# Optimization experiments

Hardware: AMD Instinct MI355X
Metric: run time of the kernel (lower is better)

## Reference

```python
import jax, jax.numpy as jnp
import numpy as np

TEMPERATURE = 0.1
EPS = 1e-8  # torch cosine_similarity eps
NEG_FILL = -9e15

def setup_inputs() -> dict:
    key = jax.random.key(0)
    stacked_batch = jax.random.normal(key, (8192, 128), dtype=jnp.float32)
    return {"stacked_batch": stacked_batch}

def reference(stacked_batch) -> jnp.ndarray:
    n = stacked_batch.shape[0]
    # cosine similarity = normalized GEMM (equivalent to torch broadcast form)
    norm = jnp.maximum(jnp.linalg.norm(stacked_batch, axis=-1, keepdims=True), EPS)
    z = stacked_batch / norm                      # [N, D]
    sim = jnp.matmul(z, z.T) / TEMPERATURE        # [N, N]
    # mask self-similarity on the diagonal
    idx = jnp.arange(n)
    sim = sim.at[idx, idx].set(NEG_FILL)
    # positive pair for row i is column (i + N/2) mod N
    pos_cols = (idx + n // 2) % n
    pos = sim[idx, pos_cols]                      # [N]
    loss = jax.scipy.special.logsumexp(sim, axis=-1) - pos
    return loss.mean()
```

## Files before the change

### kernel.cpp

```cpp
#include <hip/hip_runtime.h>
#include <hip/hip_bf16.h>

#define N 8192
#define D 128
#define HALF_N 4096
#define SQRT_SCALE_LOG2E 3.79828236f
#define LN2 0.693147180559945f

#define BLOCK_ROWS 256
#define COLS_PER_ITER 64
#define COL_SPLITS 16
#define COLS_PER_BLOCK (N / COL_SPLITS)
#define ITERS (COLS_PER_BLOCK / COLS_PER_ITER)
#define LDS_STRIDE 136

typedef short frag8 __attribute__((ext_vector_type(8)));
typedef float f32x4 __attribute__((ext_vector_type(4)));

#define OFF_POS    0
#define OFF_PSUMS  (N)
#define OFF_ACC    (N + COL_SPLITS * N)
#define OFF_CNT    (OFF_ACC + 1)
#define OFF_Z_BYTES ((OFF_ACC + 64) * 4)

__device__ __forceinline__ unsigned short f2bf(float f) {
    unsigned int u = __float_as_uint(f);
    u += 0x7FFFu + ((u >> 16) & 1u);
    return (unsigned short)(u >> 16);
}

__global__ __launch_bounds__(256) void k_normalize(const float* __restrict__ x,
                                                   unsigned short* __restrict__ z,
                                                   float* __restrict__ acc0,
                                                   unsigned int* __restrict__ counter) {
    const int row  = blockIdx.x * 4 + (threadIdx.x >> 6);
    const int lane = threadIdx.x & 63;
    float2 v = ((const float2*)x)[row * 64 + lane];
    float s = v.x * v.x + v.y * v.y;
    #pragma unroll
    for (int m = 32; m >= 1; m >>= 1) s += __shfl_xor(s, m);
    float inv = SQRT_SCALE_LOG2E / fmaxf(sqrtf(s), 1e-8f);
    ushort2 o;
    o.x = f2bf(v.x * inv);
    o.y = f2bf(v.y * inv);
    ((ushort2*)z)[row * 64 + lane] = o;
    if (blockIdx.x == 0 && threadIdx.x == 0) { acc0[0] = 0.0f; counter[0] = 0u; }
}

__global__ __launch_bounds__(256, 2) void k_simloss(const unsigned short* __restrict__ z,
                                                    float* __restrict__ psums,
                                                    float* __restrict__ pos) {
    __shared__ unsigned short lds[COLS_PER_ITER * LDS_STRIDE];

    const int tid  = threadIdx.x;
    const int wave = tid >> 6;
    const int lane = tid & 63;
    const int l15  = lane & 15;
    const int quad = lane >> 4;
    const int wrow = blockIdx.x * BLOCK_ROWS + wave * 64;
    const int colbase0 = blockIdx.y * COLS_PER_BLOCK;
    const int posbase  = (wrow + HALF_N) & (N - 1);

    const int st_r  = tid >> 4;
    const int st_c8 = tid & 15;

    frag8 a[4][4];
    #pragma unroll
    for (int s = 0; s < 4; ++s) {
        const uint4* p = (const uint4*)&z[(wrow + s * 16 + l15) * D + quad * 8];
        #pragma unroll
        for (int q = 0; q < 4; ++q) {
            uint4 t = p[q * 4];
            a[s][q] = *(frag8*)&t;
        }
    }

    float sums[4][4];
    #pragma unroll
    for (int s = 0; s < 4; ++s)
        #pragma unroll
        for (int r = 0; r < 4; ++r) sums[s][r] = 0.0f;

    uint4 t[4];
    #pragma unroll
    for (int u = 0; u < 4; ++u)
        t[u] = *(const uint4*)&z[(colbase0 + u * 16 + st_r) * D + st_c8 * 8];

    for (int it = 0; it < ITERS; ++it) {
        const int colbase = colbase0 + it * COLS_PER_ITER;
        __syncthreads();
        #pragma unroll
        for (int u = 0; u < 4; ++u)
            *(uint4*)&lds[(u * 16 + st_r) * LDS_STRIDE + st_c8 * 8] = t[u];
        __syncthreads();

        if (it + 1 < ITERS) {
            const int nb = colbase + COLS_PER_ITER;
            #pragma unroll
            for (int u = 0; u < 4; ++u)
                t[u] = *(const uint4*)&z[(nb + u * 16 + st_r) * D + st_c8 * 8];
        }

        const bool isDiag = (colbase == wrow);
        const bool isPos  = (colbase == posbase);
        const unsigned short* lp = &lds[l15 * LDS_STRIDE + quad * 8];

        #pragma unroll
        for (int c = 0; c < 4; ++c) {
            f32x4 acc[4];
            #pragma unroll
            for (int s = 0; s < 4; ++s) acc[s] = (f32x4){0.f, 0.f, 0.f, 0.f};
            #pragma unroll
            for (int q = 0; q < 4; ++q) {
                frag8 b = *(const frag8*)(lp + c * 16 * LDS_STRIDE + q * 32);
                #pragma unroll
                for (int s = 0; s < 4; ++s)
                    acc[s] = __builtin_amdgcn_mfma_f32_16x16x32_bf16(a[s][q], b, acc[s], 0, 0, 0);
            }
            if (isDiag | isPos) {
                #pragma unroll
                for (int s = 0; s < 4; ++s)
                    #pragma unroll
                    for (int r = 0; r < 4; ++r) {
                        float v = acc[s][r];
                        float e = __builtin_amdgcn_exp2f(v);
                        if (c == s) {
                            bool hit = (l15 == quad * 4 + r);
                            if (isDiag && hit) e = 0.0f;
                            if (isPos  && hit) pos[wrow + s * 16 + quad * 4 + r] = v * LN2;
                        }
                        sums[s][r] += e;
                    }
            } else {
                #pragma unroll
                for (int s = 0; s < 4; ++s)
                    #pragma unroll
                    for (int r = 0; r < 4; ++r)
                        sums[s][r] += __builtin_amdgcn_exp2f(acc[s][r]);
            }
        }
    }

    #pragma unroll
    for (int s = 0; s < 4; ++s)
        #pragma unroll
        for (int r = 0; r < 4; ++r) {
            float v = sums[s][r];
            v += __shfl_xor(v, 1);
            v += __shfl_xor(v, 2);
            v += __shfl_xor(v, 4);
            v += __shfl_xor(v, 8);
            if (l15 == 0)
                psums[blockIdx.y * N + wrow + s * 16 + quad * 4 + r] = v;
        }
}

__global__ __launch_bounds__(256) void k_rowloss(const float* __restrict__ psums,
                                                 const float* __restrict__ pos,
                                                 float* __restrict__ acc0,
                                                 unsigned int* __restrict__ counter,
                                                 float* __restrict__ out) {
    const int row = blockIdx.x * 256 + threadIdx.x;
    float t = 0.0f;
    #pragma unroll
    for (int s = 0; s < COL_SPLITS; ++s) t += psums[s * N + row];
    float loss = __logf(t) - pos[row];
    #pragma unroll
    for (int m = 32; m >= 1; m >>= 1) loss += __shfl_xor(loss, m);
    __shared__ float p[4];
    if ((threadIdx.x & 63) == 0) p[threadIdx.x >> 6] = loss;
    __syncthreads();
    if (threadIdx.x == 0) {
        atomicAdd(acc0, p[0] + p[1] + p[2] + p[3]);
        __threadfence();
        unsigned prev = atomicAdd(counter, 1u);
        if (prev == gridDim.x - 1) {
            float total = atomicAdd(acc0, 0.0f);
            out[0] = total * (1.0f / N);
        }
    }
}

extern "C" void kernel_launch(void* const* d_in, const int* in_sizes, int n_in,
                              void* d_out, int out_size, void* d_ws, size_t ws_size,
                              hipStream_t stream) {
    const float* x = (const float*)d_in[0];
    float* wsf   = (float*)d_ws;
    float* pos   = wsf + OFF_POS;
    float* psums = wsf + OFF_PSUMS;
    float* acc0  = wsf + OFF_ACC;
    unsigned int* counter = (unsigned int*)(wsf + OFF_CNT);
    unsigned short* z = (unsigned short*)((char*)d_ws + OFF_Z_BYTES);

    k_normalize<<<N / 4, 256, 0, stream>>>(x, z, acc0, counter);
    dim3 g2(N / BLOCK_ROWS, COL_SPLITS);
    k_simloss<<<g2, 256, 0, stream>>>(z, psums, pos);
    k_rowloss<<<N / 256, 256, 0, stream>>>(psums, pos, acc0, counter, (float*)d_out);
}
```

Baseline: 90.95 us.

## Exploit similarity matrix symmetry with triangular tiling and column-sum atomics

Launches only upper-triangular 256x128 tiles of the symmetric similarity matrix and accumulates both row and column exp-sums via atomics, roughly halving the GEMM and exp work. The 16-way column-split partial-sum buffer is replaced by a single atomically accumulated sum vector, zeroed in the normalize kernel. Positive logits are stored only for the first half of the rows and reused by symmetry. Adds many float atomics and drops register prefetch of the next column tile, and makes the summation order nondeterministic.

```diff
diff --git a/kernel.cpp b/kernel.cpp
--- a/kernel.cpp
+++ b/kernel.cpp
@@ -7,21 +7,18 @@
 #define SQRT_SCALE_LOG2E 3.79828236f
 #define LN2 0.693147180559945f
 
-#define BLOCK_ROWS 256
 #define COLS_PER_ITER 64
-#define COL_SPLITS 16
-#define COLS_PER_BLOCK (N / COL_SPLITS)
-#define ITERS (COLS_PER_BLOCK / COLS_PER_ITER)
+#define ITERS 2
 #define LDS_STRIDE 136
 
 typedef short frag8 __attribute__((ext_vector_type(8)));
 typedef float f32x4 __attribute__((ext_vector_type(4)));
 
-#define OFF_POS    0
-#define OFF_PSUMS  (N)
-#define OFF_ACC    (N + COL_SPLITS * N)
-#define OFF_CNT    (OFF_ACC + 1)
-#define OFF_Z_BYTES ((OFF_ACC + 64) * 4)
+#define OFF_POS 0
+#define OFF_SUM N
+#define OFF_ACC (2 * N)
+#define OFF_CNT (2 * N + 1)
+#define OFF_Z_BYTES ((2 * N + 64) * 4)
 
 __device__ __forceinline__ unsigned short f2bf(float f) {
     unsigned int u = __float_as_uint(f);
@@ -31,8 +28,7 @@
 
 __global__ __launch_bounds__(256) void k_normalize(const float* __restrict__ x,
                                                    unsigned short* __restrict__ z,
-                                                   float* __restrict__ acc0,
-                                                   unsigned int* __restrict__ counter) {
+                                                   float* __restrict__ wsf) {
     const int row  = blockIdx.x * 4 + (threadIdx.x >> 6);
     const int lane = threadIdx.x & 63;
     float2 v = ((const float2*)x)[row * 64 + lane];
@@ -44,11 +40,12 @@
     o.x = f2bf(v.x * inv);
     o.y = f2bf(v.y * inv);
     ((ushort2*)z)[row * 64 + lane] = o;
-    if (blockIdx.x == 0 && threadIdx.x == 0) { acc0[0] = 0.0f; counter[0] = 0u; }
+    const int gid = blockIdx.x * 256 + threadIdx.x;
+    if (gid < N + 2) wsf[OFF_SUM + gid] = 0.0f;
 }
 
 __global__ __launch_bounds__(256, 2) void k_simloss(const unsigned short* __restrict__ z,
-                                                    float* __restrict__ psums,
+                                                    float* __restrict__ sumexp,
                                                     float* __restrict__ pos) {
     __shared__ unsigned short lds[COLS_PER_ITER * LDS_STRIDE];
 
@@ -57,12 +54,12 @@
     const int lane = tid & 63;
     const int l15  = lane & 15;
     const int quad = lane >> 4;
-    const int wrow = blockIdx.x * BLOCK_ROWS + wave * 64;
-    const int colbase0 = blockIdx.y * COLS_PER_BLOCK;
-    const int posbase  = (wrow + HALF_N) & (N - 1);
 
-    const int st_r  = tid >> 4;
-    const int st_c8 = tid & 15;
+    int b = blockIdx.x, bi = 0;
+    while (b >= 64 - 2 * bi) { b -= 64 - 2 * bi; ++bi; }
+    const int jh = 2 * bi + b;
+    const int wrow = bi * 256 + wave * 64;
+    const int colbase0 = jh * 128;
 
     frag8 a[4][4];
     #pragma unroll
@@ -81,28 +78,24 @@
         #pragma unroll
         for (int r = 0; r < 4; ++r) sums[s][r] = 0.0f;
 
-    uint4 t[4];
-    #pragma unroll
-    for (int u = 0; u < 4; ++u)
-        t[u] = *(const uint4*)&z[(colbase0 + u * 16 + st_r) * D + st_c8 * 8];
-
     for (int it = 0; it < ITERS; ++it) {
         const int colbase = colbase0 + it * COLS_PER_ITER;
         __syncthreads();
         #pragma unroll
-        for (int u = 0; u < 4; ++u)
-            *(uint4*)&lds[(u * 16 + st_r) * LDS_STRIDE + st_c8 * 8] = t[u];
+        for (int u = 0; u < 4; ++u) {
+            int idx = u * 256 + tid;
+            int r   = idx >> 4;
+            int c8  = idx & 15;
+            uint4 t = *(const uint4*)&z[(colbase + r) * D + c8 * 8];
+            *(uint4*)&lds[r * LDS_STRIDE + c8 * 8] = t;
+        }
         __syncthreads();
 
-        if (it + 1 < ITERS) {
-            const int nb = colbase + COLS_PER_ITER;
-            #pragma unroll
-            for (int u = 0; u < 4; ++u)
-                t[u] = *(const uint4*)&z[(nb + u * 16 + st_r) * D + st_c8 * 8];
-        }
+        const bool active = (colbase >= wrow);
+        const bool isSelf = (colbase == wrow);
+        const bool isPos  = (colbase == wrow + HALF_N);
+        if (!active) continue;
 
-        const bool isDiag = (colbase == wrow);
-        const bool isPos  = (colbase == posbase);
         const unsigned short* lp = &lds[l15 * LDS_STRIDE + quad * 8];
 
         #pragma unroll
@@ -112,12 +105,13 @@
             for (int s = 0; s < 4; ++s) acc[s] = (f32x4){0.f, 0.f, 0.f, 0.f};
             #pragma unroll
             for (int q = 0; q < 4; ++q) {
-                frag8 b = *(const frag8*)(lp + c * 16 * LDS_STRIDE + q * 32);
+                frag8 bf = *(const frag8*)(lp + c * 16 * LDS_STRIDE + q * 32);
                 #pragma unroll
                 for (int s = 0; s < 4; ++s)
-                    acc[s] = __builtin_amdgcn_mfma_f32_16x16x32_bf16(a[s][q], b, acc[s], 0, 0, 0);
+                    acc[s] = __builtin_amdgcn_mfma_f32_16x16x32_bf16(a[s][q], bf, acc[s], 0, 0, 0);
             }
-            if (isDiag | isPos) {
+            float cs = 0.0f;
+            if (isSelf | isPos) {
                 #pragma unroll
                 for (int s = 0; s < 4; ++s)
                     #pragma unroll
@@ -126,17 +120,27 @@
                         float e = __builtin_amdgcn_exp2f(v);
                         if (c == s) {
                             bool hit = (l15 == quad * 4 + r);
-                            if (isDiag && hit) e = 0.0f;
+                            if (isSelf && hit) e = 0.0f;
                             if (isPos  && hit) pos[wrow + s * 16 + quad * 4 + r] = v * LN2;
                         }
                         sums[s][r] += e;
+                        cs += e;
                     }
             } else {
                 #pragma unroll
                 for (int s = 0; s < 4; ++s)
                     #pragma unroll
-                    for (int r = 0; r < 4; ++r)
-                        sums[s][r] += __builtin_amdgcn_exp2f(acc[s][r]);
+                    for (int r = 0; r < 4; ++r) {
+                        float e = __builtin_amdgcn_exp2f(acc[s][r]);
+                        sums[s][r] += e;
+                        cs += e;
+                    }
+            }
+            if (!isSelf) {
+                cs += __shfl_xor(cs, 16);
+                cs += __shfl_xor(cs, 32);
+                if (quad == 0)
+                    atomicAdd(&sumexp[colbase + c * 16 + l15], cs);
             }
         }
     }
@@ -151,20 +155,17 @@
             v += __shfl_xor(v, 4);
             v += __shfl_xor(v, 8);
             if (l15 == 0)
-                psums[blockIdx.y * N + wrow + s * 16 + quad * 4 + r] = v;
+                atomicAdd(&sumexp[wrow + s * 16 + quad * 4 + r], v);
         }
 }
 
-__global__ __launch_bounds__(256) void k_rowloss(const float* __restrict__ psums,
+__global__ __launch_bounds__(256) void k_rowloss(const float* __restrict__ sumexp,
                                                  const float* __restrict__ pos,
                                                  float* __restrict__ acc0,
                                                  unsigned int* __restrict__ counter,
                                                  float* __restrict__ out) {
     const int row = blockIdx.x * 256 + threadIdx.x;
-    float t = 0.0f;
-    #pragma unroll
-    for (int s = 0; s < COL_SPLITS; ++s) t += psums[s * N + row];
-    float loss = __logf(t) - pos[row];
+    float loss = __logf(sumexp[row]) - pos[row & (HALF_N - 1)];
     #pragma unroll
     for (int m = 32; m >= 1; m >>= 1) loss += __shfl_xor(loss, m);
     __shared__ float p[4];
@@ -185,15 +186,14 @@
                               void* d_out, int out_size, void* d_ws, size_t ws_size,
                               hipStream_t stream) {
     const float* x = (const float*)d_in[0];
-    float* wsf   = (float*)d_ws;
-    float* pos   = wsf + OFF_POS;
-    float* psums = wsf + OFF_PSUMS;
-    float* acc0  = wsf + OFF_ACC;
+    float* wsf    = (float*)d_ws;
+    float* pos    = wsf + OFF_POS;
+    float* sumexp = wsf + OFF_SUM;
+    float* acc0   = wsf + OFF_ACC;
     unsigned int* counter = (unsigned int*)(wsf + OFF_CNT);
     unsigned short* z = (unsigned short*)((char*)d_ws + OFF_Z_BYTES);
 
-    k_normalize<<<N / 4, 256, 0, stream>>>(x, z, acc0, counter);
-    dim3 g2(N / BLOCK_ROWS, COL_SPLITS);
-    k_simloss<<<g2, 256, 0, stream>>>(z, psums, pos);
-    k_rowloss<<<N / 256, 256, 0, stream>>>(psums, pos, acc0, counter, (float*)d_out);
+    k_normalize<<<N / 4, 256, 0, stream>>>(x, z, wsf);
+    k_simloss<<<1056, 256, 0, stream>>>(z, sumexp, pos);
+    k_rowloss<<<N / 256, 256, 0, stream>>>(sumexp, pos, acc0, counter, (float*)d_out);
 }
```

Result: faster. 85.60 us (-5.9%).
